# Kernel optimization log

Hardware: AMD Instinct MI355X
Metric: run time of the kernel (lower is better)

The kernel has to match this reference:

```python
import jax, jax.numpy as jnp
import numpy as np

N_NODES = 100000
N_EDGES = 800000
IN_CH = 128
HID = 128
OUT_CH = 64


def setup_inputs() -> dict:
    key = jax.random.key(0)
    ks = jax.random.split(key, 8)
    x = jax.random.normal(ks[0], (N_NODES, IN_CH), dtype=jnp.float32)
    edge_index = jax.random.randint(ks[1], (2, N_EDGES), 0, N_NODES, dtype=jnp.int64)
    # GCNConv weights (Glorot) and zero biases
    def glorot(k, fan_in, fan_out):
        s = jnp.sqrt(6.0 / (fan_in + fan_out))
        return jax.random.uniform(k, (fan_in, fan_out), jnp.float32, -s, s)
    return {
        "x": x,
        "edge_index": edge_index,
        "W1": glorot(ks[2], IN_CH, HID), "b1": jnp.zeros((HID,), jnp.float32),
        "W2": glorot(ks[3], HID, HID),   "b2": jnp.zeros((HID,), jnp.float32),
        "W3": glorot(ks[4], HID, OUT_CH), "b3": jnp.zeros((OUT_CH,), jnp.float32),
    }


def _gcn_conv(h, W, b, src, dst, norm, self_norm, n_nodes):
    """PyG GCNConv: out = D^-1/2 (A+I) D^-1/2 (h W) + b.
    Self-loop contribution added densely (self_norm = dinv^2) to avoid
    appending N extra edges."""
    h = h @ W  # [N, F_out]
    msg = h[src] * norm[:, None]  # [E, F_out] gathered + normalized messages
    agg = jax.ops.segment_sum(msg, dst, num_segments=n_nodes)
    return agg + h * self_norm[:, None] + b


def reference(x, edge_index, W1, b1, W2, b2, W3, b3):
    n_nodes = x.shape[0]
    src = edge_index[0]
    dst = edge_index[1]
    # degrees with self-loops (edge weights = 1)
    deg = jax.ops.segment_sum(jnp.ones_like(src, dtype=x.dtype), dst,
                              num_segments=n_nodes) + 1.0
    dinv = jax.lax.rsqrt(deg)
    norm = dinv[src] * dinv[dst]   # per-edge symmetric normalization
    self_norm = dinv * dinv        # normalization of the i->i self loop

    h = jax.nn.relu(_gcn_conv(x, W1, b1, src, dst, norm, self_norm, n_nodes))
    # dropout is identity in eval mode (training=False)
    h = jax.nn.relu(_gcn_conv(h, W2, b2, src, dst, norm, self_norm, n_nodes))
    out = _gcn_conv(h, W3, b3, src, dst, norm, self_norm, n_nodes)
    return out
```

## Files before the change

kernel.cpp:

```cpp
#include <hip/hip_runtime.h>


#define IN_CH 128

typedef __attribute__((ext_vector_type(8))) short bf16x8;
typedef __attribute__((ext_vector_type(4))) float f32x4;

__device__ inline unsigned short f2bf_rne(float f) {
    unsigned u = __float_as_uint(f);
    unsigned r = (u + 0x7FFFu + ((u >> 16) & 1u)) >> 16;
    return (unsigned short)r;
}
__device__ inline float bf2f(unsigned short h) {
    return __uint_as_float(((unsigned)h) << 16);
}
__device__ inline float bf2f_lo(unsigned m) {
    return __uint_as_float(m << 16);
}
__device__ inline float bf2f_hi(unsigned m) {
    return __uint_as_float(m & 0xffff0000u);
}

__global__ __launch_bounds__(256) void cnt_k(const int* __restrict__ dst,
                                             int* __restrict__ cnt, int E) {
    int e = blockIdx.x * 256 + threadIdx.x;
    if (e < E) atomicAdd(&cnt[dst[e]], 1);
}

__global__ __launch_bounds__(256) void scan1_k(const int* __restrict__ cnt,
                                               int* __restrict__ bsum,
                                               float* __restrict__ dinv, int N) {
    __shared__ int s[256];
    int tid = threadIdx.x;
    int i = blockIdx.x * 256 + tid;
    int vr = (i < N) ? cnt[i] : 0;
    if (i < N) dinv[i] = rsqrtf((float)vr + 1.0f);
    s[tid] = (i < N) ? ((vr + 8) & ~7) : 0;
    __syncthreads();
    for (int off = 128; off > 0; off >>= 1) {
        if (tid < off) s[tid] += s[tid + off];
        __syncthreads();
    }
    if (tid == 0) bsum[blockIdx.x] = s[0];
}

__global__ __launch_bounds__(512) void scan2_k(int* __restrict__ bsum, int nb) {
    __shared__ int s[512];
    __shared__ int carry_s;
    int tid = threadIdx.x;
    if (tid == 0) carry_s = 0;
    __syncthreads();
    for (int base = 0; base < nb; base += 512) {
        int c = carry_s;
        int i = base + tid;
        int v = (i < nb) ? bsum[i] : 0;
        s[tid] = v;
        __syncthreads();
        for (int off = 1; off < 512; off <<= 1) {
            int t = (tid >= off) ? s[tid - off] : 0;
            __syncthreads();
            s[tid] += t;
            __syncthreads();
        }
        if (i < nb) bsum[i] = s[tid] - v + c;
        __syncthreads();
        if (tid == 0) carry_s = c + s[511];
        __syncthreads();
    }
}

__global__ __launch_bounds__(256) void scan3_k(const int* __restrict__ cnt,
                                               const int* __restrict__ bsum,
                                               int* __restrict__ rowstart,
                                               int* __restrict__ cur, int N) {
    __shared__ int s[256];
    int tid = threadIdx.x;
    int i = blockIdx.x * 256 + tid;
    int v = (i < N) ? ((cnt[i] + 8) & ~7) : 0;
    s[tid] = v;
    __syncthreads();
    for (int off = 1; off < 256; off <<= 1) {
        int t = (tid >= off) ? s[tid - off] : 0;
        __syncthreads();
        s[tid] += t;
        __syncthreads();
    }
    if (i < N) {
        int st = s[tid] - v + bsum[blockIdx.x];
        rowstart[i] = st;
        cur[i] = st;
        if (i == N - 1) rowstart[N] = st + v;
    }
}

__device__ inline void convw_one(const float* W, unsigned short* hi, int FOUT, int id) {
    int n = id >> 7, k = id & 127;
    hi[id] = f2bf_rne(W[k * FOUT + n]);
}

__global__ __launch_bounds__(256) void fill_conv_k(
    const int* __restrict__ src, const int* __restrict__ dst,
    const float* __restrict__ dinv, int* __restrict__ cur,
    int2* __restrict__ pairs, int E, int N, int fillBlocks, int selfBlocks,
    int rangeSz,
    const float* __restrict__ W1, const float* __restrict__ W2,
    const float* __restrict__ W3,
    unsigned short* __restrict__ W1h, unsigned short* __restrict__ W2h,
    unsigned short* __restrict__ W3h) {
    if ((int)blockIdx.x < fillBlocks) {
        const int range = blockIdx.x & 7;
        const int lo = range * rangeSz;
        const int hi = lo + rangeSz;
        const int e0 = (blockIdx.x >> 3) * 1024 + threadIdx.x * 4;
        if (e0 >= E) return;
        int s[4], d[4];
        if (e0 + 4 <= E) {
            int4 s4 = *(const int4*)(src + e0);
            int4 d4 = *(const int4*)(dst + e0);
            s[0] = s4.x; s[1] = s4.y; s[2] = s4.z; s[3] = s4.w;
            d[0] = d4.x; d[1] = d4.y; d[2] = d4.z; d[3] = d4.w;
        } else {
#pragma unroll
            for (int k = 0; k < 4; ++k) {
                s[k] = (e0 + k < E) ? src[e0 + k] : 0;
                d[k] = (e0 + k < E) ? dst[e0 + k] : -1;
            }
        }
#pragma unroll
        for (int k = 0; k < 4; ++k) {
            if (d[k] >= lo && d[k] < hi) {
                float nrm = dinv[s[k]] * dinv[d[k]];
                int pos = atomicAdd(&cur[d[k]], 1);
                pairs[pos] = make_int2(s[k] * 256, __float_as_int(nrm));
            }
        }
    } else if ((int)blockIdx.x < fillBlocks + selfBlocks) {
        int i = (blockIdx.x - fillBlocks) * 256 + threadIdx.x;
        if (i < N) {
            float di = dinv[i];
            int pos = atomicAdd(&cur[i], 1);
            pairs[pos] = make_int2(i * 256, __float_as_int(di * di));
        }
    } else {
        int id = (blockIdx.x - fillBlocks - selfBlocks) * 256 + threadIdx.x;
        if (id < 16384) convw_one(W1, W1h, 128, id);
        else if (id < 32768) convw_one(W2, W2h, 128, id - 16384);
        else if (id < 40960) convw_one(W3, W3h, 64, id - 32768);
    }
}

__device__ inline bf16x8 cvt8(const float* __restrict__ p) {
    float4 v0 = *(const float4*)p;
    float4 v1 = *(const float4*)(p + 4);
    bf16x8 h;
    h[0] = (short)f2bf_rne(v0.x); h[1] = (short)f2bf_rne(v0.y);
    h[2] = (short)f2bf_rne(v0.z); h[3] = (short)f2bf_rne(v0.w);
    h[4] = (short)f2bf_rne(v1.x); h[5] = (short)f2bf_rne(v1.y);
    h[6] = (short)f2bf_rne(v1.z); h[7] = (short)f2bf_rne(v1.w);
    return h;
}

template <int FOUT, bool AF32>
__global__ __launch_bounds__(256) void mfma_gemm(const float* __restrict__ Af,
                                                 const unsigned short* __restrict__ Ahi,
                                                 const unsigned short* __restrict__ Bhi,
                                                 unsigned short* __restrict__ Thi,
                                                 int N) {
    constexpr int NCT = FOUT / 16;
    constexpr int BSTRIDE = 136;
    constexpr int CSTRIDE = FOUT + 8;
    constexpr int BU = FOUT * BSTRIDE;
    constexpr int CU = 64 * CSTRIDE;
    constexpr int SMEMU = (BU > CU) ? BU : CU;
    __shared__ unsigned short smem[SMEMU];

    const int tid = threadIdx.x;
    const int wv = tid >> 6, lane = tid & 63;
    const int quad = lane >> 4, l16 = lane & 15;
    const int row0 = blockIdx.x * 64 + wv * 16;

#pragma unroll
    for (int it = 0; it < FOUT / 16; ++it) {
        int i = it * 256 + tid;
        int r = i >> 4, c = (i & 15) * 8;
        *(bf16x8*)(&smem[r * BSTRIDE + c]) = *(const bf16x8*)(Bhi + (size_t)r * 128 + c);
    }
    __syncthreads();

    f32x4 acc[NCT];
#pragma unroll
    for (int ct = 0; ct < NCT; ++ct)
        acc[ct] = (f32x4){0.f, 0.f, 0.f, 0.f};

    const int ra = AF32 ? min(row0 + l16, N - 1) : (row0 + l16);

#pragma unroll
    for (int ks = 0; ks < 4; ++ks) {
        const int ko = ks * 32 + quad * 8;
        bf16x8 ah;
        if (AF32) {
            ah = cvt8(Af + (size_t)ra * 128 + ko);
        } else {
            ah = *(const bf16x8*)(Ahi + (size_t)ra * 128 + ko);
        }
#pragma unroll
        for (int ct = 0; ct < NCT; ++ct) {
            bf16x8 bh = *(const bf16x8*)(&smem[(ct * 16 + l16) * BSTRIDE + ko]);
            acc[ct] = __builtin_amdgcn_mfma_f32_16x16x32_bf16(ah, bh, acc[ct], 0, 0, 0);
        }
    }

    __syncthreads();
    const int lrow = wv * 16 + quad * 4;
#pragma unroll
    for (int ct = 0; ct < NCT; ++ct) {
        const int col = ct * 16 + l16;
#pragma unroll
        for (int r = 0; r < 4; ++r)
            smem[(lrow + r) * CSTRIDE + col] = f2bf_rne(acc[ct][r]);
    }
    __syncthreads();
    constexpr int CH = FOUT / 8;
#pragma unroll
    for (int i = 0; i < 64 * CH / 256; ++i) {
        int ci = i * 256 + tid;
        int r = ci / CH, c = (ci % CH) * 8;
        int grow = blockIdx.x * 64 + r;
        if (grow < N)
            *(uint4*)(Thi + (size_t)grow * FOUT + c) = *(const uint4*)&smem[r * CSTRIDE + c];
    }
}

template <int FOUT, bool SPLIT>
__global__ __launch_bounds__(256) void gather_k(const int* __restrict__ rowstart,
                                                const int2* __restrict__ pairs,
                                                const unsigned short* __restrict__ Thi,
                                                const float* __restrict__ bias,
                                                float* __restrict__ out,
                                                unsigned short* __restrict__ outHi,
                                                int N) {
    const int wave = threadIdx.x >> 6;
    const int lane = threadIdx.x & 63;
    const int row = blockIdx.x * 4 + wave;
    if (row >= N) return;

    const int start = rowstart[row];
    const int end = rowstart[row + 1];
    const char* tbase = (const char*)Thi;

    if (FOUT == 128) {
        const int laneB = lane * 4;
        float2 bb = *(const float2*)(bias + lane * 2);
        float ax = bb.x, ay = bb.y;

        int4 p0 = *(const int4*)(pairs + start);
        int4 p1 = *(const int4*)(pairs + start + 2);
        int4 p2 = *(const int4*)(pairs + start + 4);
        int4 p3 = *(const int4*)(pairs + start + 6);
        for (int j = start; j < end;) {
            const int jn = j + 8;
            unsigned m0 = *(const unsigned*)(tbase + (unsigned)p0.x + laneB);
            unsigned m1 = *(const unsigned*)(tbase + (unsigned)p0.z + laneB);
            unsigned m2 = *(const unsigned*)(tbase + (unsigned)p1.x + laneB);
            unsigned m3 = *(const unsigned*)(tbase + (unsigned)p1.z + laneB);
            unsigned m4 = *(const unsigned*)(tbase + (unsigned)p2.x + laneB);
            unsigned m5 = *(const unsigned*)(tbase + (unsigned)p2.z + laneB);
            unsigned m6 = *(const unsigned*)(tbase + (unsigned)p3.x + laneB);
            unsigned m7 = *(const unsigned*)(tbase + (unsigned)p3.z + laneB);
            int4 q0 = *(const int4*)(pairs + jn);
            int4 q1 = *(const int4*)(pairs + jn + 2);
            int4 q2 = *(const int4*)(pairs + jn + 4);
            int4 q3 = *(const int4*)(pairs + jn + 6);
            float n0 = __int_as_float(p0.y), n1 = __int_as_float(p0.w);
            float n2 = __int_as_float(p1.y), n3 = __int_as_float(p1.w);
            float n4 = __int_as_float(p2.y), n5 = __int_as_float(p2.w);
            float n6 = __int_as_float(p3.y), n7 = __int_as_float(p3.w);
            ax += n0 * bf2f_lo(m0); ay += n0 * bf2f_hi(m0);
            ax += n1 * bf2f_lo(m1); ay += n1 * bf2f_hi(m1);
            ax += n2 * bf2f_lo(m2); ay += n2 * bf2f_hi(m2);
            ax += n3 * bf2f_lo(m3); ay += n3 * bf2f_hi(m3);
            ax += n4 * bf2f_lo(m4); ay += n4 * bf2f_hi(m4);
            ax += n5 * bf2f_lo(m5); ay += n5 * bf2f_hi(m5);
            ax += n6 * bf2f_lo(m6); ay += n6 * bf2f_hi(m6);
            ax += n7 * bf2f_lo(m7); ay += n7 * bf2f_hi(m7);
            p0 = q0; p1 = q1; p2 = q2; p3 = q3;
            j = jn;
        }

        if (SPLIT) {
            ushort2 h;
            h.x = f2bf_rne(fmaxf(ax, 0.f));
            h.y = f2bf_rne(fmaxf(ay, 0.f));
            *(ushort2*)(outHi + (size_t)row * 128 + lane * 2) = h;
        } else {
            float2 o; o.x = ax; o.y = ay;
            *(float2*)(out + (size_t)row * 128 + lane * 2) = o;
        }
    } else {
        const int laneB = lane * 2;
        float acc = bias[lane];

        int4 p0 = *(const int4*)(pairs + start);
        int4 p1 = *(const int4*)(pairs + start + 2);
        int4 p2 = *(const int4*)(pairs + start + 4);
        int4 p3 = *(const int4*)(pairs + start + 6);
        for (int j = start; j < end;) {
            const int jn = j + 8;
            float m0 = bf2f(*(const unsigned short*)(tbase + ((unsigned)p0.x >> 1) + laneB));
            float m1 = bf2f(*(const unsigned short*)(tbase + ((unsigned)p0.z >> 1) + laneB));
            float m2 = bf2f(*(const unsigned short*)(tbase + ((unsigned)p1.x >> 1) + laneB));
            float m3 = bf2f(*(const unsigned short*)(tbase + ((unsigned)p1.z >> 1) + laneB));
            float m4 = bf2f(*(const unsigned short*)(tbase + ((unsigned)p2.x >> 1) + laneB));
            float m5 = bf2f(*(const unsigned short*)(tbase + ((unsigned)p2.z >> 1) + laneB));
            float m6 = bf2f(*(const unsigned short*)(tbase + ((unsigned)p3.x >> 1) + laneB));
            float m7 = bf2f(*(const unsigned short*)(tbase + ((unsigned)p3.z >> 1) + laneB));
            int4 q0 = *(const int4*)(pairs + jn);
            int4 q1 = *(const int4*)(pairs + jn + 2);
            int4 q2 = *(const int4*)(pairs + jn + 4);
            int4 q3 = *(const int4*)(pairs + jn + 6);
            acc += __int_as_float(p0.y) * m0 + __int_as_float(p0.w) * m1 +
                   __int_as_float(p1.y) * m2 + __int_as_float(p1.w) * m3 +
                   __int_as_float(p2.y) * m4 + __int_as_float(p2.w) * m5 +
                   __int_as_float(p3.y) * m6 + __int_as_float(p3.w) * m7;
            p0 = q0; p1 = q1; p2 = q2; p3 = q3;
            j = jn;
        }
        out[(size_t)row * FOUT + lane] = acc;
    }
}

extern "C" void kernel_launch(void* const* d_in, const int* in_sizes, int n_in,
                              void* d_out, int out_size, void* d_ws, size_t ws_size,
                              hipStream_t stream) {
    const float* x  = (const float*)d_in[0];
    const int* eidx = (const int*)d_in[1];
    const float* W1 = (const float*)d_in[2];
    const float* b1 = (const float*)d_in[3];
    const float* W2 = (const float*)d_in[4];
    const float* b2 = (const float*)d_in[5];
    const float* W3 = (const float*)d_in[6];
    const float* b3 = (const float*)d_in[7];
    float* out = (float*)d_out;

    const int N = in_sizes[0] / IN_CH;
    const int E = in_sizes[1] / 2;
    const int* src = eidx;
    const int* dst = eidx + E;
    const int Npad = ((N + 127) / 128) * 128;
    const int nb = (N + 255) / 256;
    const int Emax = E + 8 * N + 24;

    auto align = [](size_t v) { return (v + 255) / 256 * 256; };
    char* p = (char*)d_ws;
    int* cnt = (int*)p;            p += align((size_t)N * 4);
    int* rowstart = (int*)p;       p += align((size_t)(N + 1) * 4);
    int* cur = (int*)p;            p += align((size_t)N * 4);
    int* bsum = (int*)p;           p += align((size_t)nb * 4);
    float* dinv = (float*)p;       p += align((size_t)N * 4);
    int2* pairs = (int2*)p;        p += align((size_t)Emax * 8);
    unsigned short* Ahi = (unsigned short*)p;  p += align((size_t)Npad * 128 * 2);
    unsigned short* Thi = (unsigned short*)p;  p += align((size_t)Npad * 128 * 2);
    unsigned short* W1h = (unsigned short*)p;  p += align(128 * 128 * 2);
    unsigned short* W2h = (unsigned short*)p;  p += align(128 * 128 * 2);
    unsigned short* W3h = (unsigned short*)p;

    hipMemsetAsync(cnt, 0, (size_t)N * 4, stream);
    hipMemsetAsync(pairs, 0, (size_t)Emax * 8, stream);
    cnt_k<<<(E + 255) / 256, 256, 0, stream>>>(dst, cnt, E);
    scan1_k<<<nb, 256, 0, stream>>>(cnt, bsum, dinv, N);
    scan2_k<<<1, 512, 0, stream>>>(bsum, nb);
    scan3_k<<<nb, 256, 0, stream>>>(cnt, bsum, rowstart, cur, N);
    const int chunks = (E + 1023) / 1024;
    const int fillBlocks = chunks * 8;
    const int selfBlocks = (N + 255) / 256;
    const int rangeSz = (N + 7) / 8;
    fill_conv_k<<<fillBlocks + selfBlocks + 160, 256, 0, stream>>>(
        src, dst, dinv, cur, pairs, E, N, fillBlocks, selfBlocks, rangeSz,
        W1, W2, W3, W1h, W2h, W3h);

    const int gemm_blocks = (N + 63) / 64;
    const int gather_blocks = (N + 3) / 4;

    mfma_gemm<128, true><<<gemm_blocks, 256, 0, stream>>>(x, nullptr, W1h, Thi, N);
    gather_k<128, true><<<gather_blocks, 256, 0, stream>>>(rowstart, pairs, Thi,
                                                           b1, nullptr, Ahi, N);
    mfma_gemm<128, false><<<gemm_blocks, 256, 0, stream>>>(nullptr, Ahi, W2h, Thi, N);
    gather_k<128, true><<<gather_blocks, 256, 0, stream>>>(rowstart, pairs, Thi,
                                                           b2, nullptr, Ahi, N);
    mfma_gemm<64, false><<<gemm_blocks, 256, 0, stream>>>(nullptr, Ahi, W3h, Thi, N);
    gather_k<64, false><<<gather_blocks, 256, 0, stream>>>(rowstart, pairs, Thi,
                                                           b3, out, nullptr, N);
}
```

Before: 329.8 us.

## Process two destination rows per wave with half-wave lanes and wider loads

The gather kernel now assigns two destination rows per 64-lane wave, with each 32-lane half handling one row and loading 8 bytes (128-wide) or 4 bytes (64-wide) per lane per neighbor instead of 4 or 2. The loop runs until neither half has edges left, using an active mask so the shorter row idles. This halves the number of waves and makes each gather access wider, aiming at better memory-level parallelism and fewer instructions per edge. The cost is divergence when the two rows have different degrees, plus extra pair loads past the end of a row.

```diff
diff --git a/kernel.cpp b/kernel.cpp
--- a/kernel.cpp
+++ b/kernel.cpp
@@ -170,8 +170,8 @@
     constexpr int BSTRIDE = 136;
     constexpr int CSTRIDE = FOUT + 8;
     constexpr int BU = FOUT * BSTRIDE;
-    constexpr int CU = 64 * CSTRIDE;
-    constexpr int SMEMU = (BU > CU) ? BU : CU;
+    constexpr int CU2 = 64 * CSTRIDE;
+    constexpr int SMEMU = (BU > CU2) ? BU : CU2;
     __shared__ unsigned short smem[SMEMU];
 
     const int tid = threadIdx.x;
@@ -229,6 +229,17 @@
         if (grow < N)
             *(uint4*)(Thi + (size_t)grow * FOUT + c) = *(const uint4*)&smem[r * CSTRIDE + c];
     }
+}
+
+struct Pairs4 { int4 p0, p1, p2, p3; };
+
+__device__ inline Pairs4 ldpairs(const int2* __restrict__ pairs, int j) {
+    Pairs4 r;
+    r.p0 = *(const int4*)(pairs + j);
+    r.p1 = *(const int4*)(pairs + j + 2);
+    r.p2 = *(const int4*)(pairs + j + 4);
+    r.p3 = *(const int4*)(pairs + j + 6);
+    return r;
 }
 
 template <int FOUT, bool SPLIT>
@@ -241,91 +252,116 @@
                                                 int N) {
     const int wave = threadIdx.x >> 6;
     const int lane = threadIdx.x & 63;
-    const int row = blockIdx.x * 4 + wave;
-    if (row >= N) return;
-
-    const int start = rowstart[row];
-    const int end = rowstart[row + 1];
+    const int half = lane >> 5;
+    const int l = lane & 31;
+    const int row = blockIdx.x * 8 + wave * 2 + half;
+    const bool rowOK = row < N;
+    const int rr = rowOK ? row : (N - 1);
+
+    const int s0 = rowstart[rr];
+    const int e = rowOK ? rowstart[rr + 1] : s0;
     const char* tbase = (const char*)Thi;
 
+    int j = s0;
+    Pairs4 P = ldpairs(pairs, j);
+
     if (FOUT == 128) {
-        const int laneB = lane * 4;
-        float2 bb = *(const float2*)(bias + lane * 2);
-        float ax = bb.x, ay = bb.y;
-
-        int4 p0 = *(const int4*)(pairs + start);
-        int4 p1 = *(const int4*)(pairs + start + 2);
-        int4 p2 = *(const int4*)(pairs + start + 4);
-        int4 p3 = *(const int4*)(pairs + start + 6);
-        for (int j = start; j < end;) {
+        const int laneB = l * 8;
+        float4 bb = *(const float4*)(bias + l * 4);
+        float a0 = bb.x, a1 = bb.y, a2 = bb.z, a3 = bb.w;
+
+        for (;;) {
+            bool act = j < e;
+            if (!__any(act)) break;
+            uint2 m0 = *(const uint2*)(tbase + (unsigned)P.p0.x + laneB);
+            uint2 m1 = *(const uint2*)(tbase + (unsigned)P.p0.z + laneB);
+            uint2 m2 = *(const uint2*)(tbase + (unsigned)P.p1.x + laneB);
+            uint2 m3 = *(const uint2*)(tbase + (unsigned)P.p1.z + laneB);
+            uint2 m4 = *(const uint2*)(tbase + (unsigned)P.p2.x + laneB);
+            uint2 m5 = *(const uint2*)(tbase + (unsigned)P.p2.z + laneB);
+            uint2 m6 = *(const uint2*)(tbase + (unsigned)P.p3.x + laneB);
+            uint2 m7 = *(const uint2*)(tbase + (unsigned)P.p3.z + laneB);
             const int jn = j + 8;
-            unsigned m0 = *(const unsigned*)(tbase + (unsigned)p0.x + laneB);
-            unsigned m1 = *(const unsigned*)(tbase + (unsigned)p0.z + laneB);
-            unsigned m2 = *(const unsigned*)(tbase + (unsigned)p1.x + laneB);
-            unsigned m3 = *(const unsigned*)(tbase + (unsigned)p1.z + laneB);
-            unsigned m4 = *(const unsigned*)(tbase + (unsigned)p2.x + laneB);
-            unsigned m5 = *(const unsigned*)(tbase + (unsigned)p2.z + laneB);
-            unsigned m6 = *(const unsigned*)(tbase + (unsigned)p3.x + laneB);
-            unsigned m7 = *(const unsigned*)(tbase + (unsigned)p3.z + laneB);
-            int4 q0 = *(const int4*)(pairs + jn);
-            int4 q1 = *(const int4*)(pairs + jn + 2);
-            int4 q2 = *(const int4*)(pairs + jn + 4);
-            int4 q3 = *(const int4*)(pairs + jn + 6);
-            float n0 = __int_as_float(p0.y), n1 = __int_as_float(p0.w);
-            float n2 = __int_as_float(p1.y), n3 = __int_as_float(p1.w);
-            float n4 = __int_as_float(p2.y), n5 = __int_as_float(p2.w);
-            float n6 = __int_as_float(p3.y), n7 = __int_as_float(p3.w);
-            ax += n0 * bf2f_lo(m0); ay += n0 * bf2f_hi(m0);
-            ax += n1 * bf2f_lo(m1); ay += n1 * bf2f_hi(m1);
-            ax += n2 * bf2f_lo(m2); ay += n2 * bf2f_hi(m2);
-            ax += n3 * bf2f_lo(m3); ay += n3 * bf2f_hi(m3);
-            ax += n4 * bf2f_lo(m4); ay += n4 * bf2f_hi(m4);
-            ax += n5 * bf2f_lo(m5); ay += n5 * bf2f_hi(m5);
-            ax += n6 * bf2f_lo(m6); ay += n6 * bf2f_hi(m6);
-            ax += n7 * bf2f_lo(m7); ay += n7 * bf2f_hi(m7);
-            p0 = q0; p1 = q1; p2 = q2; p3 = q3;
-            j = jn;
-        }
-
-        if (SPLIT) {
-            ushort2 h;
-            h.x = f2bf_rne(fmaxf(ax, 0.f));
-            h.y = f2bf_rne(fmaxf(ay, 0.f));
-            *(ushort2*)(outHi + (size_t)row * 128 + lane * 2) = h;
-        } else {
-            float2 o; o.x = ax; o.y = ay;
-            *(float2*)(out + (size_t)row * 128 + lane * 2) = o;
+            Pairs4 Q = ldpairs(pairs, jn);
+            if (act) {
+                float n0 = __int_as_float(P.p0.y), n1 = __int_as_float(P.p0.w);
+                float n2 = __int_as_float(P.p1.y), n3 = __int_as_float(P.p1.w);
+                float n4 = __int_as_float(P.p2.y), n5 = __int_as_float(P.p2.w);
+                float n6 = __int_as_float(P.p3.y), n7 = __int_as_float(P.p3.w);
+                a0 += n0 * bf2f_lo(m0.x); a1 += n0 * bf2f_hi(m0.x);
+                a2 += n0 * bf2f_lo(m0.y); a3 += n0 * bf2f_hi(m0.y);
+                a0 += n1 * bf2f_lo(m1.x); a1 += n1 * bf2f_hi(m1.x);
+                a2 += n1 * bf2f_lo(m1.y); a3 += n1 * bf2f_hi(m1.y);
+                a0 += n2 * bf2f_lo(m2.x); a1 += n2 * bf2f_hi(m2.x);
+                a2 += n2 * bf2f_lo(m2.y); a3 += n2 * bf2f_hi(m2.y);
+                a0 += n3 * bf2f_lo(m3.x); a1 += n3 * bf2f_hi(m3.x);
+                a2 += n3 * bf2f_lo(m3.y); a3 += n3 * bf2f_hi(m3.y);
+                a0 += n4 * bf2f_lo(m4.x); a1 += n4 * bf2f_hi(m4.x);
+                a2 += n4 * bf2f_lo(m4.y); a3 += n4 * bf2f_hi(m4.y);
+                a0 += n5 * bf2f_lo(m5.x); a1 += n5 * bf2f_hi(m5.x);
+                a2 += n5 * bf2f_lo(m5.y); a3 += n5 * bf2f_hi(m5.y);
+                a0 += n6 * bf2f_lo(m6.x); a1 += n6 * bf2f_hi(m6.x);
+                a2 += n6 * bf2f_lo(m6.y); a3 += n6 * bf2f_hi(m6.y);
+                a0 += n7 * bf2f_lo(m7.x); a1 += n7 * bf2f_hi(m7.x);
+                a2 += n7 * bf2f_lo(m7.y); a3 += n7 * bf2f_hi(m7.y);
+                j = jn;
+            }
+            P = Q;
+        }
+
+        if (rowOK) {
+            if (SPLIT) {
+                ushort4 h;
+                h.x = f2bf_rne(fmaxf(a0, 0.f));
+                h.y = f2bf_rne(fmaxf(a1, 0.f));
+                h.z = f2bf_rne(fmaxf(a2, 0.f));
+                h.w = f2bf_rne(fmaxf(a3, 0.f));
+                *(ushort4*)(outHi + (size_t)row * 128 + l * 4) = h;
+            } else {
+                float4 o; o.x = a0; o.y = a1; o.z = a2; o.w = a3;
+                *(float4*)(out + (size_t)row * 128 + l * 4) = o;
+            }
         }
     } else {
-        const int laneB = lane * 2;
-        float acc = bias[lane];
-
-        int4 p0 = *(const int4*)(pairs + start);
-        int4 p1 = *(const int4*)(pairs + start + 2);
-        int4 p2 = *(const int4*)(pairs + start + 4);
-        int4 p3 = *(const int4*)(pairs + start + 6);
-        for (int j = start; j < end;) {
+        const int laneB = l * 4;
+        float2 bb = *(const float2*)(bias + l * 2);
+        float a0 = bb.x, a1 = bb.y;
+
+        for (;;) {
+            bool act = j < e;
+            if (!__any(act)) break;
+            unsigned m0 = *(const unsigned*)(tbase + ((unsigned)P.p0.x >> 1) + laneB);
+            unsigned m1 = *(const unsigned*)(tbase + ((unsigned)P.p0.z >> 1) + laneB);
+            unsigned m2 = *(const unsigned*)(tbase + ((unsigned)P.p1.x >> 1) + laneB);
+            unsigned m3 = *(const unsigned*)(tbase + ((unsigned)P.p1.z >> 1) + laneB);
+            unsigned m4 = *(const unsigned*)(tbase + ((unsigned)P.p2.x >> 1) + laneB);
+            unsigned m5 = *(const unsigned*)(tbase + ((unsigned)P.p2.z >> 1) + laneB);
+            unsigned m6 = *(const unsigned*)(tbase + ((unsigned)P.p3.x >> 1) + laneB);
+            unsigned m7 = *(const unsigned*)(tbase + ((unsigned)P.p3.z >> 1) + laneB);
             const int jn = j + 8;
-            float m0 = bf2f(*(const unsigned short*)(tbase + ((unsigned)p0.x >> 1) + laneB));
-            float m1 = bf2f(*(const unsigned short*)(tbase + ((unsigned)p0.z >> 1) + laneB));
-            float m2 = bf2f(*(const unsigned short*)(tbase + ((unsigned)p1.x >> 1) + laneB));
-            float m3 = bf2f(*(const unsigned short*)(tbase + ((unsigned)p1.z >> 1) + laneB));
-            float m4 = bf2f(*(const unsigned short*)(tbase + ((unsigned)p2.x >> 1) + laneB));
-            float m5 = bf2f(*(const unsigned short*)(tbase + ((unsigned)p2.z >> 1) + laneB));
-            float m6 = bf2f(*(const unsigned short*)(tbase + ((unsigned)p3.x >> 1) + laneB));
-            float m7 = bf2f(*(const unsigned short*)(tbase + ((unsigned)p3.z >> 1) + laneB));
-            int4 q0 = *(const int4*)(pairs + jn);
-            int4 q1 = *(const int4*)(pairs + jn + 2);
-            int4 q2 = *(const int4*)(pairs + jn + 4);
-            int4 q3 = *(const int4*)(pairs + jn + 6);
-            acc += __int_as_float(p0.y) * m0 + __int_as_float(p0.w) * m1 +
-                   __int_as_float(p1.y) * m2 + __int_as_float(p1.w) * m3 +
-                   __int_as_float(p2.y) * m4 + __int_as_float(p2.w) * m5 +
-                   __int_as_float(p3.y) * m6 + __int_as_float(p3.w) * m7;
-            p0 = q0; p1 = q1; p2 = q2; p3 = q3;
-            j = jn;
-        }
-        out[(size_t)row * FOUT + lane] = acc;
+            Pairs4 Q = ldpairs(pairs, jn);
+            if (act) {
+                float n0 = __int_as_float(P.p0.y), n1 = __int_as_float(P.p0.w);
+                float n2 = __int_as_float(P.p1.y), n3 = __int_as_float(P.p1.w);
+                float n4 = __int_as_float(P.p2.y), n5 = __int_as_float(P.p2.w);
+                float n6 = __int_as_float(P.p3.y), n7 = __int_as_float(P.p3.w);
+                a0 += n0 * bf2f_lo(m0); a1 += n0 * bf2f_hi(m0);
+                a0 += n1 * bf2f_lo(m1); a1 += n1 * bf2f_hi(m1);
+                a0 += n2 * bf2f_lo(m2); a1 += n2 * bf2f_hi(m2);
+                a0 += n3 * bf2f_lo(m3); a1 += n3 * bf2f_hi(m3);
+                a0 += n4 * bf2f_lo(m4); a1 += n4 * bf2f_hi(m4);
+                a0 += n5 * bf2f_lo(m5); a1 += n5 * bf2f_hi(m5);
+                a0 += n6 * bf2f_lo(m6); a1 += n6 * bf2f_hi(m6);
+                a0 += n7 * bf2f_lo(m7); a1 += n7 * bf2f_hi(m7);
+                j = jn;
+            }
+            P = Q;
+        }
+
+        if (rowOK) {
+            float2 o; o.x = a0; o.y = a1;
+            *(float2*)(out + (size_t)row * 64 + l * 2) = o;
+        }
     }
 }
 
@@ -379,7 +415,7 @@
         W1, W2, W3, W1h, W2h, W3h);
 
     const int gemm_blocks = (N + 63) / 64;
-    const int gather_blocks = (N + 3) / 4;
+    const int gather_blocks = (N + 7) / 8;
 
     mfma_gemm<128, true><<<gemm_blocks, 256, 0, stream>>>(x, nullptr, W1h, Thi, N);
     gather_k<128, true><<<gather_blocks, 256, 0, stream>>>(rowstart, pairs, Thi,
```

Measured after the change: 331.1 us. No clear change (+0.4%).
